# Kernel optimization log

Measured on AMD Instinct MI355X. Metric: run time of the kernel, lower is better.

## Reference

```python
import jax, jax.numpy as jnp
import numpy as np

B, N, M, DC, NUM_ITERS = 64, 1024, 512, 6, 5
# leave-one-out index table: row j lists the DC-1 positions != j
LOO = np.array([[k for k in range(DC) if k != j] for j in range(DC)])  # [DC, DC-1]


def setup_inputs() -> dict:
    key = jax.random.key(0)
    k1, k2, k3, k4 = jax.random.split(key, 4)
    rng = np.random.default_rng(0)
    # row-regular sparse parity-check matrix: each check touches exactly DC variables
    row_cols = np.stack([np.sort(rng.choice(N, DC, replace=False)) for _ in range(M)]).astype(np.int32)
    H = np.zeros((M, N), np.float32)
    H[np.arange(M)[:, None], row_cols] = 1.0
    soft_input = jax.random.normal(k1, (B, N), jnp.float32) * 2.0  # channel LLRs
    labels = jax.random.randint(k2, (B, N), 0, 2).astype(jnp.int64)
    # neural_network_process: Dense(4) then Dense(1), no bias, non-negative weights
    W1 = jnp.abs(jax.random.normal(k3, (DC - 1, 4), jnp.float32)) * 0.3
    W2 = jnp.abs(jax.random.normal(k4, (4, 1), jnp.float32)) * 0.3
    bit_w1 = jnp.full((1,), -0.048, jnp.float32)
    bit_w2 = jnp.full((1,), -0.048, jnp.float32)
    return dict(soft_input=soft_input, labels=labels, H=jnp.asarray(H),
                row_cols=jnp.asarray(row_cols), W1=W1, W2=W2,
                bit_w1=bit_w1, bit_w2=bit_w2)


def reference(soft_input, labels, H, row_cols, W1, W2, bit_w1, bit_w2):
    # NMS-r belief propagation: NUM_ITERS iterations of vc update, check-node
    # update via sorted leave-one-out magnitudes fed to a tiny non-neg NN,
    # and marginalization. Returns all soft outputs [NUM_ITERS+1, B, N].
    rows = jnp.arange(M)[:, None]                 # [M,1] for gather/scatter
    sp1 = jax.nn.softplus(bit_w1)                 # bit weight 1 (compute_vc)
    sp2 = jax.nn.softplus(bit_w2)                 # bit weight 2 (marginalize)
    loo = jnp.asarray(LOO)

    def body(cv, _):
        # compute_vc
        temp = cv.sum(axis=1) + soft_input * sp1  # [B,N]
        vc = temp[:, None, :] * H - cv            # [B,M,N]
        # compute_cv1: sign part
        s = jnp.sign((1.0 - H)[None] + vc)        # +1 at H==0 positions
        result_sign = jnp.prod(s, axis=-1)[..., None] * H * s
        # magnitude part: gather the DC nonzeros per check row
        nz = jnp.abs(vc)[:, rows, row_cols]       # [B,M,DC]
        srt = jnp.sort(nz[..., loo], axis=-1)     # [B,M,DC,DC-1] sorted ascending
        vals = ((srt @ W1) @ W2)[..., 0]          # tiny NN -> [B,M,DC]
        cv_dense = jnp.zeros_like(vc).at[:, rows, row_cols].set(vals)
        cv_new = jax.lax.stop_gradient(result_sign) * cv_dense
        # marginalize
        soft_out = cv_new.sum(axis=1) + sp2 * soft_input
        return cv_new, soft_out

    cv0 = jnp.zeros((soft_input.shape[0], M, N), jnp.float32)
    _, outs = jax.lax.scan(body, cv0, None, length=NUM_ITERS)
    return jnp.concatenate([soft_input[None], outs], axis=0)  # soft_output_list
```

## Files before the change

### kernel.cpp

```cpp
#include <hip/hip_runtime.h>


constexpr int BB    = 64;
constexpr int NCOL  = 1024;
constexpr int KDC   = 6;
constexpr int ITERS = 5;
constexpr int THR   = 512;
constexpr int TOT   = BB * NCOL;

__device__ __forceinline__ float softplusf(float x) {
    return fmaxf(x, 0.f) + log1pf(expf(-fabsf(x)));
}

__global__ void __launch_bounds__(THR) k_decode(
        const float* __restrict__ soft,
        const int*   __restrict__ row_cols,
        const float* __restrict__ W1,
        const float* __restrict__ W2,
        const float* __restrict__ bw1,
        const float* __restrict__ bw2,
        float* __restrict__ out) {
    __shared__ float S[3][NCOL];

    const int tid = threadIdx.x;
    const int b   = blockIdx.x;
    const int n0  = 2 * tid, n1 = 2 * tid + 1;

    const float sp1 = softplusf(bw1[0]);
    const float sp2 = softplusf(bw2[0]);
    const float dsp = sp2 - sp1;

    float w[KDC - 1];
#pragma unroll
    for (int j = 0; j < KDC - 1; ++j) {
        float a = 0.f;
#pragma unroll
        for (int q = 0; q < 4; ++q) a += W1[j * 4 + q] * W2[q];
        w[j] = a;
    }

    const float2 sv = *reinterpret_cast<const float2*>(soft + b * NCOL + n0);
    const float s0 = sv.x, s1 = sv.y;
    *reinterpret_cast<float2*>(out + b * NCOL + n0) = sv;
    const float base0 = sp1 * s0, base1 = sp1 * s1;
    S[0][n0] = base0;  S[0][n1] = base1;
    S[1][n0] = base0;  S[1][n1] = base1;

    int   cols[KDC];
    float cv[KDC];
#pragma unroll
    for (int k = 0; k < KDC; ++k) {
        cols[k] = row_cols[tid * KDC + k];
        cv[k]   = 0.f;
    }
    __syncthreads();

#pragma unroll
    for (int p = 0; p < ITERS; ++p) {
        const int rd = p % 3, ac = (p + 1) % 3, zr = (p + 2) % 3;

        float v[KDC];
#pragma unroll
        for (int k = 0; k < KDC; ++k) v[k] = S[rd][cols[k]] - cv[k];

        if (p >= 1) {
            float2 o;
            o.x = fmaf(dsp, s0, S[rd][n0]);
            o.y = fmaf(dsp, s1, S[rd][n1]);
            *reinterpret_cast<float2*>(out + (size_t)p * TOT + b * NCOL + n0) = o;
        }
        if (p < ITERS - 1) {
            S[zr][n0] = base0;  S[zr][n1] = base1;
        }

#define CE(i, j) { bool sw = fabsf(v[i]) > fabsf(v[j]);                  \
        float tv = sw ? v[j] : v[i]; v[j] = sw ? v[i] : v[j]; v[i] = tv; \
        int tc = sw ? cols[j] : cols[i];                                  \
        cols[j] = sw ? cols[i] : cols[j]; cols[i] = tc; }
        CE(0,1)
        CE(1,2) CE(0,1)
        CE(2,3) CE(1,2) CE(0,1)
        CE(3,4) CE(2,3) CE(1,2) CE(0,1)
        CE(4,5) CE(3,4) CE(2,3) CE(1,2) CE(0,1)
#undef CE

        float        mg[KDC];
        unsigned int sb[KDC];
#pragma unroll
        for (int r = 0; r < KDC; ++r) {
            mg[r] = fabsf(v[r]);
            sb[r] = __float_as_uint(v[r]) & 0x80000000u;
        }
        const unsigned int Pb = sb[0] ^ sb[1] ^ sb[2] ^ sb[3] ^ sb[4] ^ sb[5];

        float pre[KDC];
        pre[0] = 0.f;
#pragma unroll
        for (int r = 0; r < KDC - 1; ++r) pre[r + 1] = pre[r] + mg[r] * w[r];
        float suf[KDC];
        suf[KDC - 1] = 0.f;
#pragma unroll
        for (int r = KDC - 2; r >= 0; --r) suf[r] = suf[r + 1] + mg[r + 1] * w[r];

#pragma unroll
        for (int r = 0; r < KDC; ++r) {
            const float cvn = __uint_as_float(
                __float_as_uint(pre[r] + suf[r]) | (Pb ^ sb[r]));
            cv[r] = cvn;
            atomicAdd(&S[ac][cols[r]], cvn);
        }
        __syncthreads();
    }

    float2 o;
    o.x = fmaf(dsp, s0, S[ITERS % 3][n0]);
    o.y = fmaf(dsp, s1, S[ITERS % 3][n1]);
    *reinterpret_cast<float2*>(out + (size_t)ITERS * TOT + b * NCOL + n0) = o;
}

extern "C" void kernel_launch(void* const* d_in, const int* in_sizes, int n_in,
                              void* d_out, int out_size, void* d_ws, size_t ws_size,
                              hipStream_t stream) {
    const float* soft     = (const float*)d_in[0];
    const int*   row_cols = (const int*)d_in[3];
    const float* W1       = (const float*)d_in[4];
    const float* W2       = (const float*)d_in[5];
    const float* bw1      = (const float*)d_in[6];
    const float* bw2      = (const float*)d_in[7];
    float* out = (float*)d_out;

    k_decode<<<dim3(BB), dim3(THR), 0, stream>>>(soft, row_cols, W1, W2,
                                                 bw1, bw2, out);
}
```

Baseline: 91.21 us.

## Decode each codeword with a single wavefront handling eight checks per lane

Each block shrinks from 512 threads (one check per thread) to one 64-lane wavefront. Every lane now processes 8 check rows and 16 variable columns, with the row_cols reads vectorised as int4. Because only one wave touches the block's shared memory, the triple-buffered accumulator becomes a single buffer that is read, reset and accumulated in program order, and the iteration loop is no longer unrolled. The aim is to remove the cost of synchronising many waves across the block and to gain instruction-level parallelism from independent checks. The trade-offs are far fewer active waves per CU to hide LDS and atomic latency, and much higher register pressure from the 48-entry arrays.

```diff
diff --git a/kernel.cpp b/kernel.cpp
--- a/kernel.cpp
+++ b/kernel.cpp
@@ -5,14 +5,15 @@
 constexpr int NCOL  = 1024;
 constexpr int KDC   = 6;
 constexpr int ITERS = 5;
-constexpr int THR   = 512;
 constexpr int TOT   = BB * NCOL;
+constexpr int CPL   = 8;
+constexpr int JV    = 8;
 
 __device__ __forceinline__ float softplusf(float x) {
     return fmaxf(x, 0.f) + log1pf(expf(-fabsf(x)));
 }
 
-__global__ void __launch_bounds__(THR) k_decode(
+__global__ void __launch_bounds__(64, 1) k_decode(
         const float* __restrict__ soft,
         const int*   __restrict__ row_cols,
         const float* __restrict__ W1,
@@ -20,11 +21,10 @@
         const float* __restrict__ bw1,
         const float* __restrict__ bw2,
         float* __restrict__ out) {
-    __shared__ float S[3][NCOL];
+    __shared__ float S[NCOL];
 
-    const int tid = threadIdx.x;
-    const int b   = blockIdx.x;
-    const int n0  = 2 * tid, n1 = 2 * tid + 1;
+    const int l = threadIdx.x;
+    const int b = blockIdx.x;
 
     const float sp1 = softplusf(bw1[0]);
     const float sp2 = softplusf(bw2[0]);
@@ -39,83 +39,112 @@
         w[j] = a;
     }
 
-    const float2 sv = *reinterpret_cast<const float2*>(soft + b * NCOL + n0);
-    const float s0 = sv.x, s1 = sv.y;
-    *reinterpret_cast<float2*>(out + b * NCOL + n0) = sv;
-    const float base0 = sp1 * s0, base1 = sp1 * s1;
-    S[0][n0] = base0;  S[0][n1] = base1;
-    S[1][n0] = base0;  S[1][n1] = base1;
+    float2 sv[JV];
+    const float* sbp = soft + b * NCOL;
+    float* ob0 = out + b * NCOL;
+#pragma unroll
+    for (int j = 0; j < JV; ++j) {
+        const int n = 2 * l + 128 * j;
+        sv[j] = *reinterpret_cast<const float2*>(sbp + n);
+        *reinterpret_cast<float2*>(ob0 + n) = sv[j];
+        *reinterpret_cast<float2*>(&S[n]) =
+            make_float2(sp1 * sv[j].x, sp1 * sv[j].y);
+    }
 
-    int   cols[KDC];
-    float cv[KDC];
+    int   cols[CPL * KDC];
+    float cv[CPL * KDC];
+    {
+        const int4* rp = reinterpret_cast<const int4*>(row_cols) + 12 * l;
 #pragma unroll
-    for (int k = 0; k < KDC; ++k) {
-        cols[k] = row_cols[tid * KDC + k];
-        cv[k]   = 0.f;
+        for (int t = 0; t < 12; ++t) {
+            const int4 q = rp[t];
+            cols[4 * t]     = q.x;  cols[4 * t + 1] = q.y;
+            cols[4 * t + 2] = q.z;  cols[4 * t + 3] = q.w;
+        }
+#pragma unroll
+        for (int e = 0; e < CPL * KDC; ++e) cv[e] = 0.f;
     }
     __syncthreads();
 
+#pragma unroll 1
+    for (int p = 0; p < ITERS; ++p) {
+        float v[CPL * KDC];
 #pragma unroll
-    for (int p = 0; p < ITERS; ++p) {
-        const int rd = p % 3, ac = (p + 1) % 3, zr = (p + 2) % 3;
+        for (int e = 0; e < CPL * KDC; ++e) v[e] = S[cols[e]] - cv[e];
 
-        float v[KDC];
+        float2 mg[JV];
 #pragma unroll
-        for (int k = 0; k < KDC; ++k) v[k] = S[rd][cols[k]] - cv[k];
-
+        for (int j = 0; j < JV; ++j) {
+            const int n = 2 * l + 128 * j;
+            mg[j] = *reinterpret_cast<const float2*>(&S[n]);
+        }
         if (p >= 1) {
-            float2 o;
-            o.x = fmaf(dsp, s0, S[rd][n0]);
-            o.y = fmaf(dsp, s1, S[rd][n1]);
-            *reinterpret_cast<float2*>(out + (size_t)p * TOT + b * NCOL + n0) = o;
+            float* op = out + (size_t)p * TOT + b * NCOL;
+#pragma unroll
+            for (int j = 0; j < JV; ++j) {
+                const int n = 2 * l + 128 * j;
+                *reinterpret_cast<float2*>(op + n) = make_float2(
+                    fmaf(dsp, sv[j].x, mg[j].x), fmaf(dsp, sv[j].y, mg[j].y));
+            }
         }
-        if (p < ITERS - 1) {
-            S[zr][n0] = base0;  S[zr][n1] = base1;
+#pragma unroll
+        for (int j = 0; j < JV; ++j) {
+            const int n = 2 * l + 128 * j;
+            *reinterpret_cast<float2*>(&S[n]) =
+                make_float2(sp1 * sv[j].x, sp1 * sv[j].y);
         }
 
-#define CE(i, j) { bool sw = fabsf(v[i]) > fabsf(v[j]);                  \
-        float tv = sw ? v[j] : v[i]; v[j] = sw ? v[i] : v[j]; v[i] = tv; \
-        int tc = sw ? cols[j] : cols[i];                                  \
-        cols[j] = sw ? cols[i] : cols[j]; cols[i] = tc; }
-        CE(0,1)
-        CE(1,2) CE(0,1)
-        CE(2,3) CE(1,2) CE(0,1)
-        CE(3,4) CE(2,3) CE(1,2) CE(0,1)
-        CE(4,5) CE(3,4) CE(2,3) CE(1,2) CE(0,1)
+#pragma unroll
+        for (int jc = 0; jc < CPL; ++jc) {
+            const int e0 = jc * KDC;
+#define CE(i, j) { bool sw = fabsf(v[e0+(i)]) > fabsf(v[e0+(j)]);             \
+            float tv = sw ? v[e0+(j)] : v[e0+(i)];                            \
+            v[e0+(j)] = sw ? v[e0+(i)] : v[e0+(j)]; v[e0+(i)] = tv;           \
+            int tc = sw ? cols[e0+(j)] : cols[e0+(i)];                        \
+            cols[e0+(j)] = sw ? cols[e0+(i)] : cols[e0+(j)]; cols[e0+(i)] = tc; }
+            CE(0,1)
+            CE(1,2) CE(0,1)
+            CE(2,3) CE(1,2) CE(0,1)
+            CE(3,4) CE(2,3) CE(1,2) CE(0,1)
+            CE(4,5) CE(3,4) CE(2,3) CE(1,2) CE(0,1)
 #undef CE
+            float        mgv[KDC];
+            unsigned int sb[KDC];
+#pragma unroll
+            for (int r = 0; r < KDC; ++r) {
+                mgv[r] = fabsf(v[e0 + r]);
+                sb[r]  = __float_as_uint(v[e0 + r]) & 0x80000000u;
+            }
+            const unsigned int Pb = sb[0] ^ sb[1] ^ sb[2] ^ sb[3] ^ sb[4] ^ sb[5];
 
-        float        mg[KDC];
-        unsigned int sb[KDC];
+            float pre[KDC];
+            pre[0] = 0.f;
 #pragma unroll
-        for (int r = 0; r < KDC; ++r) {
-            mg[r] = fabsf(v[r]);
-            sb[r] = __float_as_uint(v[r]) & 0x80000000u;
-        }
-        const unsigned int Pb = sb[0] ^ sb[1] ^ sb[2] ^ sb[3] ^ sb[4] ^ sb[5];
-
-        float pre[KDC];
-        pre[0] = 0.f;
+            for (int r = 0; r < KDC - 1; ++r) pre[r + 1] = pre[r] + mgv[r] * w[r];
+            float suf[KDC];
+            suf[KDC - 1] = 0.f;
 #pragma unroll
-        for (int r = 0; r < KDC - 1; ++r) pre[r + 1] = pre[r] + mg[r] * w[r];
-        float suf[KDC];
-        suf[KDC - 1] = 0.f;
-#pragma unroll
-        for (int r = KDC - 2; r >= 0; --r) suf[r] = suf[r + 1] + mg[r + 1] * w[r];
+            for (int r = KDC - 2; r >= 0; --r) suf[r] = suf[r + 1] + mgv[r + 1] * w[r];
 
 #pragma unroll
-        for (int r = 0; r < KDC; ++r) {
-            const float cvn = __uint_as_float(
-                __float_as_uint(pre[r] + suf[r]) | (Pb ^ sb[r]));
-            cv[r] = cvn;
-            atomicAdd(&S[ac][cols[r]], cvn);
+            for (int r = 0; r < KDC; ++r) {
+                const float cvn = __uint_as_float(
+                    __float_as_uint(pre[r] + suf[r]) | (Pb ^ sb[r]));
+                cv[e0 + r] = cvn;
+                atomicAdd(&S[cols[e0 + r]], cvn);
+            }
         }
         __syncthreads();
     }
 
-    float2 o;
-    o.x = fmaf(dsp, s0, S[ITERS % 3][n0]);
-    o.y = fmaf(dsp, s1, S[ITERS % 3][n1]);
-    *reinterpret_cast<float2*>(out + (size_t)ITERS * TOT + b * NCOL + n0) = o;
+    float* op = out + (size_t)ITERS * TOT + b * NCOL;
+#pragma unroll
+    for (int j = 0; j < JV; ++j) {
+        const int n = 2 * l + 128 * j;
+        const float2 t = *reinterpret_cast<const float2*>(&S[n]);
+        *reinterpret_cast<float2*>(op + n) = make_float2(
+            fmaf(dsp, sv[j].x, t.x), fmaf(dsp, sv[j].y, t.y));
+    }
 }
 
 extern "C" void kernel_launch(void* const* d_in, const int* in_sizes, int n_in,
@@ -129,6 +158,6 @@
     const float* bw2      = (const float*)d_in[7];
     float* out = (float*)d_out;
 
-    k_decode<<<dim3(BB), dim3(THR), 0, stream>>>(soft, row_cols, W1, W2,
-                                                 bw1, bw2, out);
+    k_decode<<<dim3(BB), dim3(64), 0, stream>>>(soft, row_cols, W1, W2,
+                                                bw1, bw2, out);
 }
```

Result: no change. 91.43 us (+0.2%).
